# Performance work log

Measured on AMD Instinct MI355X. Metric: run time of the kernel, lower is better.

The kernel has to match this reference:

```python
import jax, jax.numpy as jnp
import numpy as np

HEADS = 8
DIM = 512
SCALE = (DIM // HEADS) ** (-0.5)  # 0.125


def setup_inputs() -> dict:
    key = jax.random.key(0)
    k1, k2, k3, k4 = jax.random.split(key, 4)
    B, C, H, W = 4, DIM, 96, 96
    x = jax.random.normal(k1, (B, C, H, W), dtype=jnp.float32)
    # 1x1 conv weights collapsed to matrices [out_ch, in_ch]
    w_qkv = jax.random.normal(k2, (3 * DIM, DIM), dtype=jnp.float32) * (DIM ** -0.5)
    w_out = jax.random.normal(k3, (DIM, DIM), dtype=jnp.float32) * (DIM ** -0.5)
    b_out = jax.random.normal(k4, (DIM,), dtype=jnp.float32) * 0.01
    return {"x": x, "w_qkv": w_qkv, "w_out": w_out, "b_out": b_out}


def reference(x, w_qkv, w_out, b_out):
    # axis='height' branch of the original forward
    b, c, h, w = x.shape
    heads = HEADS
    d = c // heads
    # 1x1 conv == per-pixel GEMM: [B,3C,H,W]
    qkv = jnp.einsum('bchw,oc->bohw', x, w_qkv)
    # 'b (qkv heads d) x y -> qkv b heads x y d'
    qkv = qkv.reshape(b, 3, heads, d, h, w)
    qkv = jnp.transpose(qkv, (1, 0, 2, 4, 5, 3))  # [3, b, heads, h, w, d]
    q, k, v = qkv[0], qkv[1], qkv[2]
    # attention along the width axis, batched over (b, heads, row x)
    dots = jnp.einsum('bhxid,bhxjd->bhxij', q, k) * SCALE
    attn = jax.nn.softmax(dots, axis=-1)
    out = jnp.einsum('bhxij,bhxjd->bhxid', attn, v)  # [b, heads, h, w, d]
    # 'b heads x y d -> b (heads d) x y'
    out = jnp.transpose(out, (0, 1, 4, 2, 3)).reshape(b, heads * d, h, w)
    # to_out 1x1 conv with bias
    out = jnp.einsum('bchw,oc->bohw', out, w_out) + b_out[None, :, None, None]
    return out
```

## Files before the change

kernel.cpp:

```cpp
#include <hip/hip_runtime.h>

typedef unsigned short u16;
typedef unsigned int u32;
typedef __attribute__((ext_vector_type(8))) short short8;
typedef __attribute__((ext_vector_type(4))) float floatx4;

#define HEADS 8
#define DIM 512
#define HH 96
#define WW 96
#define NPIX 9216
#define M_TOT 36864
#define N_QKV 1536
#define SCALE 0.125f

__device__ __forceinline__ float b2f(u16 v){
    union{float f;u32 u;}x; x.u=((u32)v)<<16; return x.f;
}
__device__ __forceinline__ u16 f2b(float f){
    union{float f;u32 u;}x; x.f=f;
    u32 u=x.u + 0x7fffu + ((x.u>>16)&1u);
    return (u16)(u>>16);
}
__device__ __forceinline__ u32 pack2(float a,float b){
    u32 r; asm("v_cvt_pk_bf16_f32 %0, %1, %2" : "=v"(r) : "v"(a), "v"(b));
    return r;
}
__device__ __forceinline__ short8 mk8(u32 a,u32 b,u32 c,u32 d){
    union{u32 u[4]; short8 v;} x; x.u[0]=a; x.u[1]=b; x.u[2]=c; x.u[3]=d; return x.v;
}

__device__ __forceinline__ void gload16(const u16* g, u16* l){
    __builtin_amdgcn_global_load_lds(
        (const __attribute__((address_space(1))) u32*)g,
        (__attribute__((address_space(3))) u32*)l, 16, 0, 0);
}

__global__ void detect_dtype(const u16* __restrict__ wq, int* __restrict__ flag){
    __shared__ int cnt;
    if (threadIdx.x==0) cnt=0;
    __syncthreads();
    u16 u = wq[2*threadIdx.x];
    int e = (u>>7)&0xff;
    if (e>=100 && e<=128) atomicAdd(&cnt,1);
    __syncthreads();
    if (threadIdx.x==0) *flag = (cnt>128)?1:0;
}

__global__ __launch_bounds__(256)
void convert_w(const void* __restrict__ wq, const void* __restrict__ wo,
               const int* __restrict__ flag, u16* __restrict__ wqb, u16* __restrict__ wob){
    const int isb = *flag;
    int i = blockIdx.x*256 + threadIdx.x;
    const int nq = N_QKV*DIM;
    if (i < nq){
        wqb[i] = isb ? ((const u16*)wq)[i] : f2b(((const float*)wq)[i]);
    } else {
        int j = i - nq;
        wob[j] = isb ? ((const u16*)wo)[j] : f2b(((const float*)wo)[j]);
    }
}

__global__ __launch_bounds__(256)
void convert_x(const void* __restrict__ xv, const int* __restrict__ flag,
               u16* __restrict__ xb){
    __shared__ u16 tile[64][65];
    const int isb = *flag;
    const int p0 = blockIdx.x*64, c0 = blockIdx.y*64, b = blockIdx.z;
    const int t = threadIdx.x;
    const int pl = t&63, c4 = t>>6;
    const float* x32 = (const float*)xv;
    const u16*   x16 = (const u16*)xv;
    size_t src = ((size_t)b*DIM + c0 + c4)*NPIX + p0 + pl;
    #pragma unroll
    for (int i=0;i<16;i++){
        int cl = c4 + i*4;
        size_t s = src + (size_t)i*4*NPIX;
        tile[cl][pl] = isb ? x16[s] : f2b(x32[s]);
    }
    __syncthreads();
    const int cu = t&31, r8 = t>>5;
    u32* xb32 = (u32*)xb;
    #pragma unroll
    for (int i=0;i<8;i++){
        int pr = r8 + i*8;
        u32 v = (u32)tile[2*cu][pr] | ((u32)tile[2*cu+1][pr]<<16);
        xb32[((size_t)b*NPIX + p0 + pr)*(DIM/2) + (c0>>1) + cu] = v;
    }
}

__global__ __launch_bounds__(512, 2)
void gemm_qkv(const u16* __restrict__ A, const u16* __restrict__ B,
              u16* __restrict__ qkt, u16* __restrict__ vtt){
    __shared__ __align__(16) union ShMem {
        u16 tiles[65536];
        float ctQ[8][16][68];
        float ctV[8][16][132];
    } sh;
    u16* lds = sh.tiles;
    const int id = blockIdx.x;
    const int xcd = id & 7, slot = id >> 3;
    const int q6 = slot/6;
    const int by = xcd*18 + q6;
    const int bx = slot - q6*6;
    const int t = threadIdx.x;
    const int w = t>>6, l = t&63, lr = l&15, lq = l>>4;
    const int wm2 = w>>2, wn4 = w&3;
    const int m0 = by*256, n0 = bx*256;
    const u16* gA0 = A + (size_t)(m0 +       w*16 + lr)*DIM + lq*8;
    const u16* gA1 = A + (size_t)(m0 + 128 + w*16 + lr)*DIM + lq*8;
    const u16* gB0 = B + (size_t)(n0 +       w*16 + lr)*DIM + lq*8;
    const u16* gB1 = B + (size_t)(n0 + 128 + w*16 + lr)*DIM + lq*8;

#define STG(gp, opb, h, ko, bb) do { \
        const u16* _g = (gp) + (ko); \
        u16* _l = lds + (bb)*32768 + (opb) + ((h)*8 + w)*1024; \
        gload16(_g,      _l); \
        gload16(_g + 32, _l + 512); \
    } while(0)

    floatx4 acc[8][4] = {};
    STG(gA0, 0,     0, 0, 0);
    STG(gA1, 0,     1, 0, 0);
    STG(gB0, 16384, 0, 0, 0);
    STG(gB1, 16384, 1, 0, 0);

    #pragma unroll 1
    for (int ktile=0; ktile<8; ++ktile){
        const int cur = ktile&1, nxt = cur^1;
        const int ko = (ktile+1)*64;
        if (ktile < 7){
            STG(gA0, 0, 0, ko, nxt);
            asm volatile("s_waitcnt vmcnt(2)" ::: "memory");
        } else {
            asm volatile("s_waitcnt vmcnt(0)" ::: "memory");
        }
        __builtin_amdgcn_s_barrier();
        asm volatile("" ::: "memory");
        const u16* bA = lds + cur*32768 +         wm2*8192 + l*8;
        const u16* bB = lds + cur*32768 + 16384 + wn4*4096 + l*8;
        short8 af[4][2], blo[2][2], bhi[2][2];
        #pragma unroll
        for (int mi=0;mi<4;mi++){
            af[mi][0] = *(const short8*)(bA + mi*1024);
            af[mi][1] = *(const short8*)(bA + mi*1024 + 512);
        }
        #pragma unroll
        for (int ni=0;ni<2;ni++){
            blo[ni][0] = *(const short8*)(bB + ni*1024);
            blo[ni][1] = *(const short8*)(bB + ni*1024 + 512);
        }
        if (ktile < 7) STG(gA1, 0, 1, ko, nxt);
        asm volatile("" ::: "memory");
        __builtin_amdgcn_s_barrier();
        __builtin_amdgcn_sched_barrier(0);
        __builtin_amdgcn_s_setprio(1);
        #pragma unroll
        for (int mi=0;mi<4;mi++)
            #pragma unroll
            for (int ni=0;ni<2;ni++){
                acc[mi][ni] = __builtin_amdgcn_mfma_f32_16x16x32_bf16(af[mi][0], blo[ni][0], acc[mi][ni], 0,0,0);
                acc[mi][ni] = __builtin_amdgcn_mfma_f32_16x16x32_bf16(af[mi][1], blo[ni][1], acc[mi][ni], 0,0,0);
            }
        __builtin_amdgcn_s_setprio(0);
        __builtin_amdgcn_sched_barrier(0);
        __builtin_amdgcn_s_barrier();
        #pragma unroll
        for (int ni=0;ni<2;ni++){
            bhi[ni][0] = *(const short8*)(bB + (2+ni)*1024);
            bhi[ni][1] = *(const short8*)(bB + (2+ni)*1024 + 512);
        }
        if (ktile < 7) STG(gB0, 16384, 0, ko, nxt);
        asm volatile("" ::: "memory");
        __builtin_amdgcn_s_barrier();
        __builtin_amdgcn_sched_barrier(0);
        __builtin_amdgcn_s_setprio(1);
        #pragma unroll
        for (int mi=0;mi<4;mi++)
            #pragma unroll
            for (int ni=0;ni<2;ni++){
                acc[mi][2+ni] = __builtin_amdgcn_mfma_f32_16x16x32_bf16(af[mi][0], bhi[ni][0], acc[mi][2+ni], 0,0,0);
                acc[mi][2+ni] = __builtin_amdgcn_mfma_f32_16x16x32_bf16(af[mi][1], bhi[ni][1], acc[mi][2+ni], 0,0,0);
            }
        __builtin_amdgcn_s_setprio(0);
        __builtin_amdgcn_sched_barrier(0);
        __builtin_amdgcn_s_barrier();
        #pragma unroll
        for (int mi=0;mi<4;mi++){
            af[mi][0] = *(const short8*)(bA + (4+mi)*1024);
            af[mi][1] = *(const short8*)(bA + (4+mi)*1024 + 512);
        }
        if (ktile < 7) STG(gB1, 16384, 1, ko, nxt);
        asm volatile("" ::: "memory");
        __builtin_amdgcn_s_barrier();
        __builtin_amdgcn_sched_barrier(0);
        __builtin_amdgcn_s_setprio(1);
        #pragma unroll
        for (int mi=0;mi<4;mi++)
            #pragma unroll
            for (int ni=0;ni<2;ni++){
                acc[4+mi][2+ni] = __builtin_amdgcn_mfma_f32_16x16x32_bf16(af[mi][0], bhi[ni][0], acc[4+mi][2+ni], 0,0,0);
                acc[4+mi][2+ni] = __builtin_amdgcn_mfma_f32_16x16x32_bf16(af[mi][1], bhi[ni][1], acc[4+mi][2+ni], 0,0,0);
            }
        __builtin_amdgcn_s_setprio(0);
        __builtin_amdgcn_sched_barrier(0);
        __builtin_amdgcn_s_barrier();
        __builtin_amdgcn_s_setprio(1);
        #pragma unroll
        for (int mi=0;mi<4;mi++)
            #pragma unroll
            for (int ni=0;ni<2;ni++){
                acc[4+mi][ni] = __builtin_amdgcn_mfma_f32_16x16x32_bf16(af[mi][0], blo[ni][0], acc[4+mi][ni], 0,0,0);
                acc[4+mi][ni] = __builtin_amdgcn_mfma_f32_16x16x32_bf16(af[mi][1], blo[ni][1], acc[4+mi][ni], 0,0,0);
            }
        __builtin_amdgcn_s_setprio(0);
        __builtin_amdgcn_sched_barrier(0);
        asm volatile("" ::: "memory");
        __builtin_amdgcn_s_barrier();
        asm volatile("" ::: "memory");
    }
#undef STG
    const int bat   = m0 / NPIX;
    const int p0img = (m0 - bat*NPIX) + wm2*128;
    if (bx < 4){
        float (*ct)[68] = sh.ctQ[w];
        const int nbase = n0 + wn4*64;
        const int isK   = (nbase >= 512);
        const int head  = (nbase - (isK ? 512 : 0)) >> 6;
        const int kqoff = isK ? 6144 : 0;
        const size_t blk0 = (size_t)(bat*8 + head)*96;
        #pragma unroll
        for (int mi=0;mi<8;mi++){
            #pragma unroll
            for (int ni=0;ni<4;ni++)
                #pragma unroll
                for (int r=0;r<4;r++)
                    ct[lq*4+r][ni*16+lr] = acc[mi][ni][r];
            int pv  = (p0img + mi*16) >> 4;
            int row = pv/6, mt = pv - row*6;
            u16* dst = qkt + (blk0 + row)*12288 + kqoff + mt*1024 + l*8;
            #pragma unroll
            for (int ks=0;ks<2;ks++){
                const float* cp = &ct[l&15][ks*32 + (l>>4)*8];
                float4 v0 = *(const float4*)(cp);
                float4 v1 = *(const float4*)(cp+4);
                uint4 s;
                s.x=pack2(v0.x,v0.y); s.y=pack2(v0.z,v0.w);
                s.z=pack2(v1.x,v1.y); s.w=pack2(v1.z,v1.w);
                *((uint4*)(dst + ks*512)) = s;
            }
        }
    } else {
        float (*ct)[132] = sh.ctV[w];
        const int head = ((n0 - 1024) + wn4*64) >> 6;
        const size_t blk0 = (size_t)(bat*8 + head)*96;
        for (int ni=0; ni<4; ni++){
            #pragma unroll
            for (int mi=0;mi<8;mi++)
                #pragma unroll
                for (int r=0;r<4;r++)
                    ct[lr][mi*16 + lq*4 + r] = acc[mi][ni][r];
            #pragma unroll
            for (int cc=0;cc<4;cc++){
                int p32 = (p0img + cc*32) >> 5;
                int row = p32/3, jt = p32 - row*3;
                const float* cp = &ct[l&15][cc*32 + (l>>4)*8];
                float4 v0 = *(const float4*)(cp);
                float4 v1 = *(const float4*)(cp+4);
                uint4 s;
                s.x=pack2(v0.x,v0.y); s.y=pack2(v0.z,v0.w);
                s.z=pack2(v1.x,v1.y); s.w=pack2(v1.z,v1.w);
                *((uint4*)(vtt + (blk0 + row)*6144 + (ni*3 + jt)*512 + l*8)) = s;
            }
        }
    }
}

__global__ __launch_bounds__(256)
void attn_kernel(const u16* __restrict__ qkt, const u16* __restrict__ vtt,
                 u16* __restrict__ attno){
    const int t = threadIdx.x;
    const int w = t>>6, l = t&63, lr = l&15, lq = l>>4;
    const int id  = blockIdx.x;
    const int bid = (id&7)*576 + (id>>3);
    const int widx = bid*4 + w;
    const int qt   = widx % 6;
    const int rowu = widx / 6;
    const int row  = rowu % HH;
    const int bh   = rowu / HH;
    const int head = bh & 7, bat = bh >> 3;
    const u16* qkb = qkt + (size_t)rowu*12288;
    const u16* vb  = vtt + (size_t)rowu*6144;
    short8 qf0 = *(const short8*)(qkb + (qt*2+0)*512 + l*8);
    short8 qf1 = *(const short8*)(qkb + (qt*2+1)*512 + l*8);
    floatx4 s[6];
    #pragma unroll
    for (int jt=0;jt<6;jt++){
        short8 k0 = *(const short8*)(qkb + 6144 + (jt*2+0)*512 + l*8);
        short8 k1 = *(const short8*)(qkb + 6144 + (jt*2+1)*512 + l*8);
        floatx4 a = {};
        a = __builtin_amdgcn_mfma_f32_16x16x32_bf16(k0, qf0, a, 0,0,0);
        a = __builtin_amdgcn_mfma_f32_16x16x32_bf16(k1, qf1, a, 0,0,0);
        s[jt] = a;
    }
    float m = -1e30f;
    #pragma unroll
    for (int jt=0;jt<6;jt++)
        #pragma unroll
        for (int r=0;r<4;r++){ s[jt][r] *= SCALE; m = fmaxf(m, s[jt][r]); }
    m = fmaxf(m, __shfl_xor(m, 16));
    m = fmaxf(m, __shfl_xor(m, 32));
    float sum = 0.f;
    u32 pk0[6], pk1[6];
    #pragma unroll
    for (int jt=0;jt<6;jt++){
        float e0 = __expf(s[jt][0]-m), e1 = __expf(s[jt][1]-m);
        float e2 = __expf(s[jt][2]-m), e3 = __expf(s[jt][3]-m);
        sum += e0+e1+e2+e3;
        pk0[jt] = pack2(e0,e1);
        pk1[jt] = pack2(e2,e3);
    }
    sum += __shfl_xor(sum, 16);
    sum += __shfl_xor(sum, 32);
    const float rinv = 1.f/sum;
    const int srcA = lr + ((lq&1)<<5);
    const int srcB = srcA + 16;
    const int hi   = lq>>1;
    short8 pf[3];
    #pragma unroll
    for (int kb=0;kb<3;kb++){
        u32 x0=__shfl(pk0[kb*2],srcA), y0=__shfl(pk0[kb*2+1],srcA);
        u32 x1=__shfl(pk1[kb*2],srcA), y1=__shfl(pk1[kb*2+1],srcA);
        u32 x2=__shfl(pk0[kb*2],srcB), y2=__shfl(pk0[kb*2+1],srcB);
        u32 x3=__shfl(pk1[kb*2],srcB), y3=__shfl(pk1[kb*2+1],srcB);
        pf[kb] = mk8(hi?y0:x0, hi?y1:x1, hi?y2:x2, hi?y3:x3);
    }
    floatx4 o[4] = {};
    #pragma unroll
    for (int kb=0;kb<3;kb++){
        #pragma unroll
        for (int dt=0;dt<4;dt++){
            short8 vf = *(const short8*)(vb + (dt*3+kb)*512 + l*8);
            o[dt] = __builtin_amdgcn_mfma_f32_16x16x32_bf16(vf, pf[kb], o[dt], 0,0,0);
        }
    }
    const size_t pixrow = (size_t)bat*NPIX + row*WW + qt*16;
    u16* ob = attno + (pixrow + lr)*512 + head*64 + lq*4;
    #pragma unroll
    for (int dt=0;dt<4;dt++){
        uint2 st;
        st.x = pack2(o[dt][0]*rinv, o[dt][1]*rinv);
        st.y = pack2(o[dt][2]*rinv, o[dt][3]*rinv);
        *(uint2*)(ob + dt*16) = st;
    }
}

__global__ __launch_bounds__(256, 2)
void gemm_out(const u16* __restrict__ A, const u16* __restrict__ B,
              const void* __restrict__ bias, const int* __restrict__ flag,
              void* __restrict__ outv){
    __shared__ __align__(16) union ShMem {
        u16 tiles[32768];
        float ct[4][16][68];
    } sh;
    u16* lds = sh.tiles;
    const int id = blockIdx.x;
    const int xcd = id & 7, slot = id >> 3;
    const int by = xcd*36 + (slot>>2);
    const int bx = slot & 3;
    const int t = threadIdx.x;
    const int w = t>>6, l = t&63, lr = l&15, lq = l>>4;
    const int wm = w>>1, wn = w&1;
    const int m0 = by*128, n0 = bx*128;
    const u16* gA = A + (size_t)(m0 + w*16 + lr)*DIM + lq*8;
    const u16* gB = B + (size_t)(n0 + w*16 + lr)*DIM + lq*8;

#define STG_A(h, ko, bb) do { \
        const u16* _g = gA + (size_t)(h)*32768 + (ko); \
        u16* _l = lds + (bb)*16384 + ((h)*4 + w)*1024; \
        gload16(_g,      _l); \
        gload16(_g + 32, _l + 512); \
    } while(0)
#define STG_B(h, ko, bb) do { \
        const u16* _g = gB + (size_t)(h)*32768 + (ko); \
        u16* _l = lds + (bb)*16384 + 8192 + ((h)*4 + w)*1024; \
        gload16(_g,      _l); \
        gload16(_g + 32, _l + 512); \
    } while(0)

    floatx4 acc[4][4] = {};
    STG_A(0,0,0); STG_A(1,0,0); STG_B(0,0,0); STG_B(1,0,0);

    #pragma unroll 1
    for (int kt=0; kt<8; ++kt){
        const int cur = kt&1, nxt = cur^1;
        const int ko = (kt+1)*64;
        if (kt < 7){
            STG_A(0, ko, nxt);
            asm volatile("s_waitcnt vmcnt(2)" ::: "memory");
        } else {
            asm volatile("s_waitcnt vmcnt(0)" ::: "memory");
        }
        __builtin_amdgcn_s_barrier();
        asm volatile("" ::: "memory");
        const u16* bA = lds + cur*16384 +        wm*4096 + l*8;
        const u16* bB = lds + cur*16384 + 8192 + wn*4096 + l*8;
        short8 af[4][2], bf[2][2];
        #pragma unroll
        for (int mi=0;mi<4;mi++){
            af[mi][0] = *(const short8*)(bA + mi*1024);
            af[mi][1] = *(const short8*)(bA + mi*1024 + 512);
        }
        #pragma unroll
        for (int ni=0;ni<2;ni++){
            bf[ni][0] = *(const short8*)(bB + ni*1024);
            bf[ni][1] = *(const short8*)(bB + ni*1024 + 512);
        }
        if (kt < 7) STG_A(1, ko, nxt);
        asm volatile("" ::: "memory");
        __builtin_amdgcn_s_barrier();
        __builtin_amdgcn_sched_barrier(0);
        __builtin_amdgcn_s_setprio(1);
        #pragma unroll
        for (int mi=0;mi<4;mi++)
            #pragma unroll
            for (int ni=0;ni<2;ni++){
                acc[mi][ni] = __builtin_amdgcn_mfma_f32_16x16x32_bf16(af[mi][0], bf[ni][0], acc[mi][ni], 0,0,0);
                acc[mi][ni] = __builtin_amdgcn_mfma_f32_16x16x32_bf16(af[mi][1], bf[ni][1], acc[mi][ni], 0,0,0);
            }
        __builtin_amdgcn_s_setprio(0);
        __builtin_amdgcn_sched_barrier(0);
        __builtin_amdgcn_s_barrier();
        #pragma unroll
        for (int ni=0;ni<2;ni++){
            bf[ni][0] = *(const short8*)(bB + (2+ni)*1024);
            bf[ni][1] = *(const short8*)(bB + (2+ni)*1024 + 512);
        }
        if (kt < 7){ STG_B(0, ko, nxt); STG_B(1, ko, nxt); }
        asm volatile("" ::: "memory");
        __builtin_amdgcn_s_barrier();
        __builtin_amdgcn_sched_barrier(0);
        __builtin_amdgcn_s_setprio(1);
        #pragma unroll
        for (int mi=0;mi<4;mi++)
            #pragma unroll
            for (int ni=0;ni<2;ni++){
                acc[mi][2+ni] = __builtin_amdgcn_mfma_f32_16x16x32_bf16(af[mi][0], bf[ni][0], acc[mi][2+ni], 0,0,0);
                acc[mi][2+ni] = __builtin_amdgcn_mfma_f32_16x16x32_bf16(af[mi][1], bf[ni][1], acc[mi][2+ni], 0,0,0);
            }
        __builtin_amdgcn_s_setprio(0);
        __builtin_amdgcn_sched_barrier(0);
        asm volatile("" ::: "memory");
        __builtin_amdgcn_s_barrier();
        asm volatile("" ::: "memory");
    }
#undef STG_A
#undef STG_B
    const int isb = *flag;
    const int bat  = m0 / NPIX;
    const int pix0 = (m0 - bat*NPIX) + wm*64;
    float (*ct)[68] = sh.ct[w];
    const u16*   b16 = (const u16*)bias;
    const float* b32 = (const float*)bias;
    const int nl = l>>2, seg = l&3;
    for (int ni=0; ni<4; ni++){
        #pragma unroll
        for (int mi=0;mi<4;mi++)
            #pragma unroll
            for (int r=0;r<4;r++)
                ct[lr][mi*16 + lq*4 + r] = acc[mi][ni][r];
        int ng = n0 + wn*64 + ni*16 + nl;
        float bv = isb ? b2f(b16[ng]) : b32[ng];
        const float* cp = &ct[nl][seg*16];
        float4 v0 = *(const float4*)(cp);
        float4 v1 = *(const float4*)(cp+4);
        float4 v2 = *(const float4*)(cp+8);
        float4 v3 = *(const float4*)(cp+12);
        v0.x+=bv; v0.y+=bv; v0.z+=bv; v0.w+=bv;
        v1.x+=bv; v1.y+=bv; v1.z+=bv; v1.w+=bv;
        v2.x+=bv; v2.y+=bv; v2.z+=bv; v2.w+=bv;
        v3.x+=bv; v3.y+=bv; v3.z+=bv; v3.w+=bv;
        size_t off = ((size_t)(bat*DIM + ng))*NPIX + pix0 + seg*16;
        if (isb){
            uint4 s0, s1;
            s0.x=pack2(v0.x,v0.y); s0.y=pack2(v0.z,v0.w);
            s0.z=pack2(v1.x,v1.y); s0.w=pack2(v1.z,v1.w);
            s1.x=pack2(v2.x,v2.y); s1.y=pack2(v2.z,v2.w);
            s1.z=pack2(v3.x,v3.y); s1.w=pack2(v3.z,v3.w);
            *(uint4*)((u16*)outv + off)     = s0;
            *(uint4*)((u16*)outv + off + 8) = s1;
        } else {
            float* of = (float*)outv + off;
            *(float4*)(of)    = v0;
            *(float4*)(of+4)  = v1;
            *(float4*)(of+8)  = v2;
            *(float4*)(of+12) = v3;
        }
    }
}

extern "C" void kernel_launch(void* const* d_in, const int* in_sizes, int n_in,
                              void* d_out, int out_size, void* d_ws, size_t ws_size,
                              hipStream_t stream){
    const void* x    = d_in[0];
    const void* wqkv = d_in[1];
    const void* wout = d_in[2];
    const void* bout = d_in[3];
    char* wsb = (char*)d_ws;
    int* flag    = (int*)wsb;
    u16* xb      = (u16*)(wsb + 256);
    u16* attn_ws = xb;
    u16* wqb     = xb + (size_t)M_TOT*DIM;
    u16* wob     = wqb + (size_t)N_QKV*DIM;
    u16* qk_ws   = wob + (size_t)DIM*DIM;
    u16* vt_ws   = qk_ws + (size_t)M_TOT*1024;
    detect_dtype<<<1, 256, 0, stream>>>((const u16*)wqkv, flag);
    convert_w<<<4096, 256, 0, stream>>>(wqkv, wout, flag, wqb, wob);
    convert_x<<<dim3(144, 8, 4), 256, 0, stream>>>(x, flag, xb);
    gemm_qkv<<<864, 512, 0, stream>>>(xb, wqb, qk_ws, vt_ws);
    attn_kernel<<<4608, 256, 0, stream>>>(qk_ws, vt_ws, attn_ws);
    gemm_out<<<1152, 256, 0, stream>>>(attn_ws, wob, bout, flag, d_out);
}
```

Baseline: 323.8 us.

## Fuse QKV projection GEMM with row attention into one kernel

```diff
diff --git a/kernel.cpp b/kernel.cpp
--- a/kernel.cpp
+++ b/kernel.cpp
@@ -89,269 +89,180 @@
     }
 }
 
-__global__ __launch_bounds__(512, 2)
-void gemm_qkv(const u16* __restrict__ A, const u16* __restrict__ B,
-              u16* __restrict__ qkt, u16* __restrict__ vtt){
-    __shared__ __align__(16) union ShMem {
-        u16 tiles[65536];
-        float ctQ[8][16][68];
-        float ctV[8][16][132];
-    } sh;
-    u16* lds = sh.tiles;
-    const int id = blockIdx.x;
-    const int xcd = id & 7, slot = id >> 3;
-    const int q6 = slot/6;
-    const int by = xcd*18 + q6;
-    const int bx = slot - q6*6;
-    const int t = threadIdx.x;
-    const int w = t>>6, l = t&63, lr = l&15, lq = l>>4;
-    const int wm2 = w>>2, wn4 = w&3;
-    const int m0 = by*256, n0 = bx*256;
-    const u16* gA0 = A + (size_t)(m0 +       w*16 + lr)*DIM + lq*8;
-    const u16* gA1 = A + (size_t)(m0 + 128 + w*16 + lr)*DIM + lq*8;
-    const u16* gB0 = B + (size_t)(n0 +       w*16 + lr)*DIM + lq*8;
-    const u16* gB1 = B + (size_t)(n0 + 128 + w*16 + lr)*DIM + lq*8;
-
-#define STG(gp, opb, h, ko, bb) do { \
-        const u16* _g = (gp) + (ko); \
-        u16* _l = lds + (bb)*32768 + (opb) + ((h)*8 + w)*1024; \
-        gload16(_g,      _l); \
-        gload16(_g + 32, _l + 512); \
-    } while(0)
-
-    floatx4 acc[8][4] = {};
-    STG(gA0, 0,     0, 0, 0);
-    STG(gA1, 0,     1, 0, 0);
-    STG(gB0, 16384, 0, 0, 0);
-    STG(gB1, 16384, 1, 0, 0);
-
-    #pragma unroll 1
-    for (int ktile=0; ktile<8; ++ktile){
-        const int cur = ktile&1, nxt = cur^1;
-        const int ko = (ktile+1)*64;
-        if (ktile < 7){
-            STG(gA0, 0, 0, ko, nxt);
-            asm volatile("s_waitcnt vmcnt(2)" ::: "memory");
-        } else {
-            asm volatile("s_waitcnt vmcnt(0)" ::: "memory");
-        }
-        __builtin_amdgcn_s_barrier();
-        asm volatile("" ::: "memory");
-        const u16* bA = lds + cur*32768 +         wm2*8192 + l*8;
-        const u16* bB = lds + cur*32768 + 16384 + wn4*4096 + l*8;
-        short8 af[4][2], blo[2][2], bhi[2][2];
-        #pragma unroll
-        for (int mi=0;mi<4;mi++){
-            af[mi][0] = *(const short8*)(bA + mi*1024);
-            af[mi][1] = *(const short8*)(bA + mi*1024 + 512);
-        }
-        #pragma unroll
-        for (int ni=0;ni<2;ni++){
-            blo[ni][0] = *(const short8*)(bB + ni*1024);
-            blo[ni][1] = *(const short8*)(bB + ni*1024 + 512);
-        }
-        if (ktile < 7) STG(gA1, 0, 1, ko, nxt);
-        asm volatile("" ::: "memory");
-        __builtin_amdgcn_s_barrier();
-        __builtin_amdgcn_sched_barrier(0);
-        __builtin_amdgcn_s_setprio(1);
-        #pragma unroll
-        for (int mi=0;mi<4;mi++)
-            #pragma unroll
-            for (int ni=0;ni<2;ni++){
-                acc[mi][ni] = __builtin_amdgcn_mfma_f32_16x16x32_bf16(af[mi][0], blo[ni][0], acc[mi][ni], 0,0,0);
-                acc[mi][ni] = __builtin_amdgcn_mfma_f32_16x16x32_bf16(af[mi][1], blo[ni][1], acc[mi][ni], 0,0,0);
-            }
-        __builtin_amdgcn_s_setprio(0);
-        __builtin_amdgcn_sched_barrier(0);
-        __builtin_amdgcn_s_barrier();
-        #pragma unroll
-        for (int ni=0;ni<2;ni++){
-            bhi[ni][0] = *(const short8*)(bB + (2+ni)*1024);
-            bhi[ni][1] = *(const short8*)(bB + (2+ni)*1024 + 512);
-        }
-        if (ktile < 7) STG(gB0, 16384, 0, ko, nxt);
-        asm volatile("" ::: "memory");
-        __builtin_amdgcn_s_barrier();
-        __builtin_amdgcn_sched_barrier(0);
-        __builtin_amdgcn_s_setprio(1);
-        #pragma unroll
-        for (int mi=0;mi<4;mi++)
-            #pragma unroll
-            for (int ni=0;ni<2;ni++){
-                acc[mi][2+ni] = __builtin_amdgcn_mfma_f32_16x16x32_bf16(af[mi][0], bhi[ni][0], acc[mi][2+ni], 0,0,0);
-                acc[mi][2+ni] = __builtin_amdgcn_mfma_f32_16x16x32_bf16(af[mi][1], bhi[ni][1], acc[mi][2+ni], 0,0,0);
-            }
-        __builtin_amdgcn_s_setprio(0);
-        __builtin_amdgcn_sched_barrier(0);
-        __builtin_amdgcn_s_barrier();
-        #pragma unroll
-        for (int mi=0;mi<4;mi++){
-            af[mi][0] = *(const short8*)(bA + (4+mi)*1024);
-            af[mi][1] = *(const short8*)(bA + (4+mi)*1024 + 512);
-        }
-        if (ktile < 7) STG(gB1, 16384, 1, ko, nxt);
-        asm volatile("" ::: "memory");
-        __builtin_amdgcn_s_barrier();
-        __builtin_amdgcn_sched_barrier(0);
-        __builtin_amdgcn_s_setprio(1);
-        #pragma unroll
-        for (int mi=0;mi<4;mi++)
-            #pragma unroll
-            for (int ni=0;ni<2;ni++){
-                acc[4+mi][2+ni] = __builtin_amdgcn_mfma_f32_16x16x32_bf16(af[mi][0], bhi[ni][0], acc[4+mi][2+ni], 0,0,0);
-                acc[4+mi][2+ni] = __builtin_amdgcn_mfma_f32_16x16x32_bf16(af[mi][1], bhi[ni][1], acc[4+mi][2+ni], 0,0,0);
-            }
-        __builtin_amdgcn_s_setprio(0);
-        __builtin_amdgcn_sched_barrier(0);
-        __builtin_amdgcn_s_barrier();
-        __builtin_amdgcn_s_setprio(1);
-        #pragma unroll
-        for (int mi=0;mi<4;mi++)
-            #pragma unroll
-            for (int ni=0;ni<2;ni++){
-                acc[4+mi][ni] = __builtin_amdgcn_mfma_f32_16x16x32_bf16(af[mi][0], blo[ni][0], acc[4+mi][ni], 0,0,0);
-                acc[4+mi][ni] = __builtin_amdgcn_mfma_f32_16x16x32_bf16(af[mi][1], blo[ni][1], acc[4+mi][ni], 0,0,0);
-            }
-        __builtin_amdgcn_s_setprio(0);
-        __builtin_amdgcn_sched_barrier(0);
-        asm volatile("" ::: "memory");
-        __builtin_amdgcn_s_barrier();
-        asm volatile("" ::: "memory");
-    }
-#undef STG
-    const int bat   = m0 / NPIX;
-    const int p0img = (m0 - bat*NPIX) + wm2*128;
-    if (bx < 4){
-        float (*ct)[68] = sh.ctQ[w];
-        const int nbase = n0 + wn4*64;
-        const int isK   = (nbase >= 512);
-        const int head  = (nbase - (isK ? 512 : 0)) >> 6;
-        const int kqoff = isK ? 6144 : 0;
-        const size_t blk0 = (size_t)(bat*8 + head)*96;
-        #pragma unroll
-        for (int mi=0;mi<8;mi++){
-            #pragma unroll
-            for (int ni=0;ni<4;ni++)
-                #pragma unroll
-                for (int r=0;r<4;r++)
-                    ct[lq*4+r][ni*16+lr] = acc[mi][ni][r];
-            int pv  = (p0img + mi*16) >> 4;
-            int row = pv/6, mt = pv - row*6;
-            u16* dst = qkt + (blk0 + row)*12288 + kqoff + mt*1024 + l*8;
-            #pragma unroll
-            for (int ks=0;ks<2;ks++){
-                const float* cp = &ct[l&15][ks*32 + (l>>4)*8];
-                float4 v0 = *(const float4*)(cp);
-                float4 v1 = *(const float4*)(cp+4);
-                uint4 s;
-                s.x=pack2(v0.x,v0.y); s.y=pack2(v0.z,v0.w);
-                s.z=pack2(v1.x,v1.y); s.w=pack2(v1.z,v1.w);
-                *((uint4*)(dst + ks*512)) = s;
-            }
-        }
-    } else {
-        float (*ct)[132] = sh.ctV[w];
-        const int head = ((n0 - 1024) + wn4*64) >> 6;
-        const size_t blk0 = (size_t)(bat*8 + head)*96;
-        for (int ni=0; ni<4; ni++){
-            #pragma unroll
-            for (int mi=0;mi<8;mi++)
-                #pragma unroll
-                for (int r=0;r<4;r++)
-                    ct[lr][mi*16 + lq*4 + r] = acc[mi][ni][r];
-            #pragma unroll
-            for (int cc=0;cc<4;cc++){
-                int p32 = (p0img + cc*32) >> 5;
-                int row = p32/3, jt = p32 - row*3;
-                const float* cp = &ct[l&15][cc*32 + (l>>4)*8];
-                float4 v0 = *(const float4*)(cp);
-                float4 v1 = *(const float4*)(cp+4);
-                uint4 s;
-                s.x=pack2(v0.x,v0.y); s.y=pack2(v0.z,v0.w);
-                s.z=pack2(v1.x,v1.y); s.w=pack2(v1.z,v1.w);
-                *((uint4*)(vtt + (blk0 + row)*6144 + (ni*3 + jt)*512 + l*8)) = s;
-            }
-        }
-    }
-}
-
-__global__ __launch_bounds__(256)
-void attn_kernel(const u16* __restrict__ qkt, const u16* __restrict__ vtt,
-                 u16* __restrict__ attno){
+__global__ __launch_bounds__(384, 3)
+void qkv_attn(const u16* __restrict__ xb, const u16* __restrict__ wqb,
+              u16* __restrict__ attno){
+    __shared__ __align__(16) u16 lds[36864];
     const int t = threadIdx.x;
     const int w = t>>6, l = t&63, lr = l&15, lq = l>>4;
     const int id  = blockIdx.x;
-    const int bid = (id&7)*576 + (id>>3);
-    const int widx = bid*4 + w;
-    const int qt   = widx % 6;
-    const int rowu = widx / 6;
-    const int row  = rowu % HH;
-    const int bh   = rowu / HH;
-    const int head = bh & 7, bat = bh >> 3;
-    const u16* qkb = qkt + (size_t)rowu*12288;
-    const u16* vb  = vtt + (size_t)rowu*6144;
-    short8 qf0 = *(const short8*)(qkb + (qt*2+0)*512 + l*8);
-    short8 qf1 = *(const short8*)(qkb + (qt*2+1)*512 + l*8);
-    floatx4 s[6];
-    #pragma unroll
-    for (int jt=0;jt<6;jt++){
-        short8 k0 = *(const short8*)(qkb + 6144 + (jt*2+0)*512 + l*8);
-        short8 k1 = *(const short8*)(qkb + 6144 + (jt*2+1)*512 + l*8);
-        floatx4 a = {};
-        a = __builtin_amdgcn_mfma_f32_16x16x32_bf16(k0, qf0, a, 0,0,0);
-        a = __builtin_amdgcn_mfma_f32_16x16x32_bf16(k1, qf1, a, 0,0,0);
-        s[jt] = a;
-    }
-    float m = -1e30f;
-    #pragma unroll
-    for (int jt=0;jt<6;jt++)
-        #pragma unroll
-        for (int r=0;r<4;r++){ s[jt][r] *= SCALE; m = fmaxf(m, s[jt][r]); }
-    m = fmaxf(m, __shfl_xor(m, 16));
-    m = fmaxf(m, __shfl_xor(m, 32));
-    float sum = 0.f;
-    u32 pk0[6], pk1[6];
-    #pragma unroll
-    for (int jt=0;jt<6;jt++){
-        float e0 = __expf(s[jt][0]-m), e1 = __expf(s[jt][1]-m);
-        float e2 = __expf(s[jt][2]-m), e3 = __expf(s[jt][3]-m);
-        sum += e0+e1+e2+e3;
-        pk0[jt] = pack2(e0,e1);
-        pk1[jt] = pack2(e2,e3);
-    }
-    sum += __shfl_xor(sum, 16);
-    sum += __shfl_xor(sum, 32);
-    const float rinv = 1.f/sum;
-    const int srcA = lr + ((lq&1)<<5);
-    const int srcB = srcA + 16;
-    const int hi   = lq>>1;
-    short8 pf[3];
-    #pragma unroll
-    for (int kb=0;kb<3;kb++){
-        u32 x0=__shfl(pk0[kb*2],srcA), y0=__shfl(pk0[kb*2+1],srcA);
-        u32 x1=__shfl(pk1[kb*2],srcA), y1=__shfl(pk1[kb*2+1],srcA);
-        u32 x2=__shfl(pk0[kb*2],srcB), y2=__shfl(pk0[kb*2+1],srcB);
-        u32 x3=__shfl(pk1[kb*2],srcB), y3=__shfl(pk1[kb*2+1],srcB);
-        pf[kb] = mk8(hi?y0:x0, hi?y1:x1, hi?y2:x2, hi?y3:x3);
-    }
-    floatx4 o[4] = {};
-    #pragma unroll
-    for (int kb=0;kb<3;kb++){
+    const int xcd = id & 7, s = id >> 3;
+    const int rowid = (s>>3)*8 + xcd;
+    const int head  = s & 7;
+    const int bat = rowid / HH, row = rowid % HH;
+    const int sub0 = w*2, sub1 = w*2+1;
+    const u16* gA0k = xb + ((size_t)bat*NPIX + row*WW + w*16 + lr)*DIM + lq*8;
+    const u16* gB00 = wqb + (size_t)((sub0>>2)*512 + head*64 + (sub0&3)*16 + lr)*DIM + lq*8;
+    const u16* gB10 = wqb + (size_t)((sub1>>2)*512 + head*64 + (sub1&3)*16 + lr)*DIM + lq*8;
+    const int la0 = (w*2+0)*512, la1 = (w*2+1)*512;
+    const int lb0 = 6144 + (w*4+0)*512, lb1 = 6144 + (w*4+1)*512;
+    const int lb2 = 6144 + (w*4+2)*512, lb3 = 6144 + (w*4+3)*512;
+
+#define STGALL(ko, bb) do { \
+        u16* Lb = lds + (bb)*18432 + l*8; \
+        gload16(gA0k      + (ko), Lb + la0); \
+        gload16(gA0k + 32 + (ko), Lb + la1); \
+        gload16(gB00      + (ko), Lb + lb0); \
+        gload16(gB00 + 32 + (ko), Lb + lb1); \
+        gload16(gB10      + (ko), Lb + lb2); \
+        gload16(gB10 + 32 + (ko), Lb + lb3); \
+    } while(0)
+
+    floatx4 acc[6][2] = {};
+    STGALL(0, 0);
+    #pragma unroll 1
+    for (int kt=0; kt<8; ++kt){
+        const int cur = kt&1, nxt = cur^1;
+        const int ko = (kt+1)*64;
+        if (kt < 7){
+            STGALL(ko, nxt);
+            asm volatile("s_waitcnt vmcnt(6)" ::: "memory");
+        } else {
+            asm volatile("s_waitcnt vmcnt(0)" ::: "memory");
+        }
+        __builtin_amdgcn_s_barrier();
+        asm volatile("" ::: "memory");
+        const u16* bufc = lds + cur*18432;
+        short8 bf00 = *(const short8*)&bufc[lb0 + l*8];
+        short8 bf01 = *(const short8*)&bufc[lb1 + l*8];
+        short8 bf10 = *(const short8*)&bufc[lb2 + l*8];
+        short8 bf11 = *(const short8*)&bufc[lb3 + l*8];
+        __builtin_amdgcn_s_setprio(1);
+        #pragma unroll
+        for (int mi=0;mi<6;mi++){
+            short8 a0 = *(const short8*)&bufc[(mi*2+0)*512 + l*8];
+            short8 a1 = *(const short8*)&bufc[(mi*2+1)*512 + l*8];
+            acc[mi][0] = __builtin_amdgcn_mfma_f32_16x16x32_bf16(a0, bf00, acc[mi][0], 0,0,0);
+            acc[mi][0] = __builtin_amdgcn_mfma_f32_16x16x32_bf16(a1, bf01, acc[mi][0], 0,0,0);
+            acc[mi][1] = __builtin_amdgcn_mfma_f32_16x16x32_bf16(a0, bf10, acc[mi][1], 0,0,0);
+            acc[mi][1] = __builtin_amdgcn_mfma_f32_16x16x32_bf16(a1, bf11, acc[mi][1], 0,0,0);
+        }
+        __builtin_amdgcn_s_setprio(0);
+        asm volatile("" ::: "memory");
+        __builtin_amdgcn_s_barrier();
+        asm volatile("" ::: "memory");
+    }
+#undef STGALL
+    __syncthreads();
+    float* sw = (float*)(lds + 18432 + w*1152);
+    if (w < 4){
+        const int h = w&1;
+        u16* cbase = lds + (w>>1)*6144;
+        #pragma unroll
+        for (int mi=0;mi<6;mi++){
+            #pragma unroll
+            for (int ni=0;ni<2;ni++)
+                #pragma unroll
+                for (int r=0;r<4;r++)
+                    sw[(lq*4+r)*36 + ni*16 + lr] = acc[mi][ni][r];
+            const float* cp = &sw[lr*36 + lq*8];
+            float4 v0 = *(const float4*)cp;
+            float4 v1 = *(const float4*)(cp+4);
+            uint4 sv;
+            sv.x = pack2(v0.x,v0.y); sv.y = pack2(v0.z,v0.w);
+            sv.z = pack2(v1.x,v1.y); sv.w = pack2(v1.z,v1.w);
+            *(uint4*)(cbase + (mi*2 + h)*512 + l*8) = sv;
+        }
+    } else {
+        const int h = w&1;
+        u16* cbase = lds + 12288;
+        #pragma unroll
+        for (int ni=0;ni<2;ni++){
+            #pragma unroll
+            for (int jt=0;jt<3;jt++){
+                #pragma unroll
+                for (int m2=0;m2<2;m2++)
+                    #pragma unroll
+                    for (int r=0;r<4;r++)
+                        sw[lr*36 + m2*16 + lq*4 + r] = acc[jt*2+m2][ni][r];
+                const float* cp = &sw[lr*36 + lq*8];
+                float4 v0 = *(const float4*)cp;
+                float4 v1 = *(const float4*)(cp+4);
+                uint4 sv;
+                sv.x = pack2(v0.x,v0.y); sv.y = pack2(v0.z,v0.w);
+                sv.z = pack2(v1.x,v1.y); sv.w = pack2(v1.z,v1.w);
+                *(uint4*)(cbase + ((h*2+ni)*3 + jt)*512 + l*8) = sv;
+            }
+        }
+    }
+    __syncthreads();
+    {
+        const int qt = w;
+        const u16* qc = lds;
+        const u16* kc = lds + 6144;
+        const u16* vc = lds + 12288;
+        short8 qf0 = *(const short8*)&qc[(qt*2+0)*512 + l*8];
+        short8 qf1 = *(const short8*)&qc[(qt*2+1)*512 + l*8];
+        floatx4 sa[6];
+        #pragma unroll
+        for (int jt=0;jt<6;jt++){
+            short8 k0 = *(const short8*)&kc[(jt*2+0)*512 + l*8];
+            short8 k1 = *(const short8*)&kc[(jt*2+1)*512 + l*8];
+            floatx4 a = {};
+            a = __builtin_amdgcn_mfma_f32_16x16x32_bf16(k0, qf0, a, 0,0,0);
+            a = __builtin_amdgcn_mfma_f32_16x16x32_bf16(k1, qf1, a, 0,0,0);
+            sa[jt] = a;
+        }
+        float m = -1e30f;
+        #pragma unroll
+        for (int jt=0;jt<6;jt++)
+            #pragma unroll
+            for (int r=0;r<4;r++){ sa[jt][r] *= SCALE; m = fmaxf(m, sa[jt][r]); }
+        m = fmaxf(m, __shfl_xor(m, 16));
+        m = fmaxf(m, __shfl_xor(m, 32));
+        float sum = 0.f;
+        u32 pk0[6], pk1[6];
+        #pragma unroll
+        for (int jt=0;jt<6;jt++){
+            float e0 = __expf(sa[jt][0]-m), e1 = __expf(sa[jt][1]-m);
+            float e2 = __expf(sa[jt][2]-m), e3 = __expf(sa[jt][3]-m);
+            sum += e0+e1+e2+e3;
+            pk0[jt] = pack2(e0,e1);
+            pk1[jt] = pack2(e2,e3);
+        }
+        sum += __shfl_xor(sum, 16);
+        sum += __shfl_xor(sum, 32);
+        const float rinv = 1.f/sum;
+        const int srcA = lr + ((lq&1)<<5);
+        const int srcB = srcA + 16;
+        const int hi   = lq>>1;
+        short8 pf[3];
+        #pragma unroll
+        for (int kb=0;kb<3;kb++){
+            u32 x0=__shfl(pk0[kb*2],srcA), y0=__shfl(pk0[kb*2+1],srcA);
+            u32 x1=__shfl(pk1[kb*2],srcA), y1=__shfl(pk1[kb*2+1],srcA);
+            u32 x2=__shfl(pk0[kb*2],srcB), y2=__shfl(pk0[kb*2+1],srcB);
+            u32 x3=__shfl(pk1[kb*2],srcB), y3=__shfl(pk1[kb*2+1],srcB);
+            pf[kb] = mk8(hi?y0:x0, hi?y1:x1, hi?y2:x2, hi?y3:x3);
+        }
+        floatx4 o[4] = {};
+        #pragma unroll
+        for (int kb=0;kb<3;kb++){
+            #pragma unroll
+            for (int dt=0;dt<4;dt++){
+                short8 vf = *(const short8*)&vc[(dt*3+kb)*512 + l*8];
+                o[dt] = __builtin_amdgcn_mfma_f32_16x16x32_bf16(vf, pf[kb], o[dt], 0,0,0);
+            }
+        }
+        const size_t pixrow = (size_t)bat*NPIX + row*WW + qt*16;
+        u16* ob = attno + (pixrow + lr)*512 + head*64 + lq*4;
         #pragma unroll
         for (int dt=0;dt<4;dt++){
-            short8 vf = *(const short8*)(vb + (dt*3+kb)*512 + l*8);
-            o[dt] = __builtin_amdgcn_mfma_f32_16x16x32_bf16(vf, pf[kb], o[dt], 0,0,0);
-        }
-    }
-    const size_t pixrow = (size_t)bat*NPIX + row*WW + qt*16;
-    u16* ob = attno + (pixrow + lr)*512 + head*64 + lq*4;
-    #pragma unroll
-    for (int dt=0;dt<4;dt++){
-        uint2 st;
-        st.x = pack2(o[dt][0]*rinv, o[dt][1]*rinv);
-        st.y = pack2(o[dt][2]*rinv, o[dt][3]*rinv);
-        *(uint2*)(ob + dt*16) = st;
+            uint2 st;
+            st.x = pack2(o[dt][0]*rinv, o[dt][1]*rinv);
+            st.y = pack2(o[dt][2]*rinv, o[dt][3]*rinv);
+            *(uint2*)(ob + dt*16) = st;
+        }
     }
 }
 
@@ -509,15 +420,12 @@
     char* wsb = (char*)d_ws;
     int* flag    = (int*)wsb;
     u16* xb      = (u16*)(wsb + 256);
-    u16* attn_ws = xb;
     u16* wqb     = xb + (size_t)M_TOT*DIM;
     u16* wob     = wqb + (size_t)N_QKV*DIM;
-    u16* qk_ws   = wob + (size_t)DIM*DIM;
-    u16* vt_ws   = qk_ws + (size_t)M_TOT*1024;
+    u16* attn_ws = wob + (size_t)DIM*DIM;
     detect_dtype<<<1, 256, 0, stream>>>((const u16*)wqkv, flag);
     convert_w<<<4096, 256, 0, stream>>>(wqkv, wout, flag, wqb, wob);
     convert_x<<<dim3(144, 8, 4), 256, 0, stream>>>(x, flag, xb);
-    gemm_qkv<<<864, 512, 0, stream>>>(xb, wqb, qk_ws, vt_ws);
-    attn_kernel<<<4608, 256, 0, stream>>>(qk_ws, vt_ws, attn_ws);
+    qkv_attn<<<3072, 384, 0, stream>>>(xb, wqb, attn_ws);
     gemm_out<<<1152, 256, 0, stream>>>(attn_ws, wob, bout, flag, d_out);
 }
```

Result: slower. 353.0 us (+9.0%).

## Fuse dtype detection and conversions into one vectorized preprocessing kernel

Applied to the files above, without the earlier changes.

```diff
diff --git a/kernel.cpp b/kernel.cpp
--- a/kernel.cpp
+++ b/kernel.cpp
@@ -36,56 +36,77 @@
         (__attribute__((address_space(3))) u32*)l, 16, 0, 0);
 }
 
-__global__ void detect_dtype(const u16* __restrict__ wq, int* __restrict__ flag){
-    __shared__ int cnt;
-    if (threadIdx.x==0) cnt=0;
-    __syncthreads();
-    u16 u = wq[2*threadIdx.x];
-    int e = (u>>7)&0xff;
-    if (e>=100 && e<=128) atomicAdd(&cnt,1);
-    __syncthreads();
-    if (threadIdx.x==0) *flag = (cnt>128)?1:0;
+__device__ __forceinline__ int detect_isb(const u16* wq16, int l){
+    int cnt = 0;
+    #pragma unroll
+    for (int j=0;j<4;j++){
+        u16 u = wq16[2*(l*4+j)];
+        int e = (u>>7)&0xff;
+        cnt += __popcll(__ballot(e>=100 && e<=128));
+    }
+    return cnt>128;
 }
 
 __global__ __launch_bounds__(256)
-void convert_w(const void* __restrict__ wq, const void* __restrict__ wo,
-               const int* __restrict__ flag, u16* __restrict__ wqb, u16* __restrict__ wob){
-    const int isb = *flag;
-    int i = blockIdx.x*256 + threadIdx.x;
-    const int nq = N_QKV*DIM;
-    if (i < nq){
-        wqb[i] = isb ? ((const u16*)wq)[i] : f2b(((const float*)wq)[i]);
+void convert_all(const void* __restrict__ xv, const void* __restrict__ wq,
+                 const void* __restrict__ wo, u16* __restrict__ xb,
+                 u16* __restrict__ wqb, u16* __restrict__ wob){
+    const int t = threadIdx.x;
+    const int isb = detect_isb((const u16*)wq, t&63);
+    const int id = blockIdx.x;
+    if (id < 4608){
+        __shared__ __align__(16) u32 tu[64][33];
+        const int px = id % 144, rem = id/144;
+        const int cy = rem & 7, bz = rem >> 3;
+        const int p0 = px*64, c0 = cy*64;
+        const float* x32 = (const float*)xv;
+        const u16*   x16 = (const u16*)xv;
+        const int cA = t>>4, pA = (t&15)*4;
+        #pragma unroll
+        for (int i=0;i<4;i++){
+            int cl = cA + i*16;
+            size_t s = ((size_t)bz*DIM + c0 + cl)*NPIX + p0 + pA;
+            u32 w0, w1;
+            if (isb){
+                uint2 v = *(const uint2*)(x16 + s);
+                w0 = v.x; w1 = v.y;
+            } else {
+                float4 v = *(const float4*)(x32 + s);
+                w0 = pack2(v.x, v.y); w1 = pack2(v.z, v.w);
+            }
+            tu[cl][(pA>>1)]   = w0;
+            tu[cl][(pA>>1)+1] = w1;
+        }
+        __syncthreads();
+        const int pr = t>>2, seg = t&3;
+        const int ph = pr>>1, po = pr&1;
+        u32 o[8];
+        #pragma unroll
+        for (int j=0;j<8;j++){
+            u32 a = tu[seg*16 + 2*j][ph];
+            u32 b = tu[seg*16 + 2*j + 1][ph];
+            o[j] = po ? ((a>>16) | (b & 0xffff0000u))
+                      : ((a & 0xffffu) | (b<<16));
+        }
+        u32* dst = (u32*)xb + ((size_t)bz*NPIX + p0 + pr)*256 + (c0>>1) + seg*8;
+        *(uint4*)(dst)   = make_uint4(o[0],o[1],o[2],o[3]);
+        *(uint4*)(dst+4) = make_uint4(o[4],o[5],o[6],o[7]);
     } else {
-        int j = i - nq;
-        wob[j] = isb ? ((const u16*)wo)[j] : f2b(((const float*)wo)[j]);
-    }
-}
-
-__global__ __launch_bounds__(256)
-void convert_x(const void* __restrict__ xv, const int* __restrict__ flag,
-               u16* __restrict__ xb){
-    __shared__ u16 tile[64][65];
-    const int isb = *flag;
-    const int p0 = blockIdx.x*64, c0 = blockIdx.y*64, b = blockIdx.z;
-    const int t = threadIdx.x;
-    const int pl = t&63, c4 = t>>6;
-    const float* x32 = (const float*)xv;
-    const u16*   x16 = (const u16*)xv;
-    size_t src = ((size_t)b*DIM + c0 + c4)*NPIX + p0 + pl;
-    #pragma unroll
-    for (int i=0;i<16;i++){
-        int cl = c4 + i*4;
-        size_t s = src + (size_t)i*4*NPIX;
-        tile[cl][pl] = isb ? x16[s] : f2b(x32[s]);
-    }
-    __syncthreads();
-    const int cu = t&31, r8 = t>>5;
-    u32* xb32 = (u32*)xb;
-    #pragma unroll
-    for (int i=0;i<8;i++){
-        int pr = r8 + i*8;
-        u32 v = (u32)tile[2*cu][pr] | ((u32)tile[2*cu+1][pr]<<16);
-        xb32[((size_t)b*NPIX + p0 + pr)*(DIM/2) + (c0>>1) + cu] = v;
+        int i4 = (id - 4608)*1024 + t*4;
+        const int nq = N_QKV*DIM;
+        u32 w0, w1;
+        if (i4 < nq){
+            if (isb){ uint2 v = *(const uint2*)((const u16*)wq + i4); w0=v.x; w1=v.y; }
+            else    { float4 v = *(const float4*)((const float*)wq + i4);
+                      w0=pack2(v.x,v.y); w1=pack2(v.z,v.w); }
+            *(uint2*)(wqb + i4) = make_uint2(w0,w1);
+        } else {
+            int j4 = i4 - nq;
+            if (isb){ uint2 v = *(const uint2*)((const u16*)wo + j4); w0=v.x; w1=v.y; }
+            else    { float4 v = *(const float4*)((const float*)wo + j4);
+                      w0=pack2(v.x,v.y); w1=pack2(v.z,v.w); }
+            *(uint2*)(wob + j4) = make_uint2(w0,w1);
+        }
     }
 }
 
@@ -357,7 +378,7 @@
 
 __global__ __launch_bounds__(256, 2)
 void gemm_out(const u16* __restrict__ A, const u16* __restrict__ B,
-              const void* __restrict__ bias, const int* __restrict__ flag,
+              const void* __restrict__ wqkv, const void* __restrict__ bias,
               void* __restrict__ outv){
     __shared__ __align__(16) union ShMem {
         u16 tiles[32768];
@@ -370,6 +391,7 @@
     const int bx = slot & 3;
     const int t = threadIdx.x;
     const int w = t>>6, l = t&63, lr = l&15, lq = l>>4;
+    const int isb = detect_isb((const u16*)wqkv, l);
     const int wm = w>>1, wn = w&1;
     const int m0 = by*128, n0 = bx*128;
     const u16* gA = A + (size_t)(m0 + w*16 + lr)*DIM + lq*8;
@@ -456,7 +478,6 @@
     }
 #undef STG_A
 #undef STG_B
-    const int isb = *flag;
     const int bat  = m0 / NPIX;
     const int pix0 = (m0 - bat*NPIX) + wm*64;
     float (*ct)[68] = sh.ct[w];
@@ -507,17 +528,14 @@
     const void* wout = d_in[2];
     const void* bout = d_in[3];
     char* wsb = (char*)d_ws;
-    int* flag    = (int*)wsb;
     u16* xb      = (u16*)(wsb + 256);
     u16* attn_ws = xb;
     u16* wqb     = xb + (size_t)M_TOT*DIM;
     u16* wob     = wqb + (size_t)N_QKV*DIM;
     u16* qk_ws   = wob + (size_t)DIM*DIM;
     u16* vt_ws   = qk_ws + (size_t)M_TOT*1024;
-    detect_dtype<<<1, 256, 0, stream>>>((const u16*)wqkv, flag);
-    convert_w<<<4096, 256, 0, stream>>>(wqkv, wout, flag, wqb, wob);
-    convert_x<<<dim3(144, 8, 4), 256, 0, stream>>>(x, flag, xb);
+    convert_all<<<5632, 256, 0, stream>>>(x, wqkv, wout, xb, wqb, wob);
     gemm_qkv<<<864, 512, 0, stream>>>(xb, wqb, qk_ws, vt_ws);
     attn_kernel<<<4608, 256, 0, stream>>>(qk_ws, vt_ws, attn_ws);
-    gemm_out<<<1152, 256, 0, stream>>>(attn_ws, wob, bout, flag, d_out);
-}
+    gemm_out<<<1152, 256, 0, stream>>>(attn_ws, wob, wqkv, bout, d_out);
+}
```

Result: faster. 310.8 us, median of 2 (-4.0%).
